# Performance work log

Hardware: AMD Instinct MI355X
Metric: run time of the kernel (lower is better)

## Reference

```python
import jax, jax.numpy as jnp
import numpy as np

LAM_CONSIST = 0.1
LAM_LR = 1.0
LAM_PAIR = 1.0


def _cubic(x, a=-0.75):
    # PyTorch bicubic kernel (a = -0.75)
    ax = jnp.abs(x)
    ax2 = ax * ax
    ax3 = ax2 * ax
    f1 = (a + 2.0) * ax3 - (a + 3.0) * ax2 + 1.0
    f2 = a * ax3 - 5.0 * a * ax2 + 8.0 * a * ax - 4.0 * a
    return jnp.where(ax <= 1.0, f1, jnp.where(ax < 2.0, f2, 0.0))


def _resize_matrix(in_size: int, out_size: int) -> jnp.ndarray:
    """Weight matrix [out_size, in_size] for antialiased bicubic resize
    (align_corners=False, antialias=True, border replicate) as in
    F.interpolate(..., mode='bicubic', antialias=True)."""
    scale = in_size / out_size
    s_aa = max(scale, 1.0)  # widen kernel when downscaling (antialias)
    support = 2.0 * s_aa
    ext = int(np.ceil(support)) + 1
    centers = (np.arange(out_size, dtype=np.float64) + 0.5) * scale - 0.5
    idx = np.arange(-ext, in_size + ext)
    dist = (idx[None, :] - centers[:, None]) / s_aa  # [out, in+2ext]
    w = _cubic(jnp.asarray(dist, dtype=jnp.float32))
    w = w / jnp.sum(w, axis=1, keepdims=True)  # torch normalizes window weights
    idx_c = np.clip(idx, 0, in_size - 1)  # clamp -> replicate border
    M = jnp.zeros((out_size, in_size), dtype=jnp.float32).at[:, idx_c].add(w)
    return M


def _resize_bicubic_aa(img: jnp.ndarray, th: int, tw: int) -> jnp.ndarray:
    # img: [B, C, H, W] -> [B, C, th, tw], separable resize via two matmuls
    _, _, h, w = img.shape
    Mh = _resize_matrix(h, th)  # [th, h]
    Mw = _resize_matrix(w, tw)  # [tw, w]
    return jnp.einsum('oh,bchw,pw->bcop', Mh, img, Mw)


def setup_inputs() -> dict:
    key = jax.random.key(0)
    k1, k2, k3 = jax.random.split(key, 3)
    pred_hr = jax.random.normal(k1, (32, 3, 512, 512), dtype=jnp.float32)
    target_hr = jax.random.normal(k2, (32, 3, 512, 512), dtype=jnp.float32)
    lr_ref = jax.random.normal(k3, (32, 3, 128, 128), dtype=jnp.float32)
    scale = jnp.full((32,), 4.0, dtype=jnp.float32)  # uniform -> static sizes
    return {"pred_hr": pred_hr, "target_hr": target_hr, "lr_ref": lr_ref, "scale": scale}


def reference(pred_hr, target_hr, lr_ref, scale):
    pix = jnp.mean(jnp.abs(pred_hr - target_hr))
    # project_scale(pred_hr, src=scale, dst=1): uniform scale=4 ->
    # target size == lr_ref spatial size (static, read from lr_ref shape)
    th, tw = lr_ref.shape[-2], lr_ref.shape[-1]
    pred_lr = _resize_bicubic_aa(pred_hr, th, tw)
    lr_term = jnp.mean(jnp.abs(pred_lr - lr_ref))
    pair_term = jnp.float32(0.0)  # pair_pred_hr / pair_scale are None
    consist = LAM_LR * lr_term + LAM_PAIR * pair_term
    total = pix + LAM_CONSIST * consist
    return (total, pix, consist, lr_term, pair_term)
```

## Files before the change

### kernel.cpp

```cpp
#include <hip/hip_runtime.h>

#define HW    512
#define OUTW  128
#define NIMG  96
#define N_HR  ((long long)NIMG*HW*HW)
#define N_LR  ((long long)NIMG*OUTW*OUTW)
#define NPART (NIMG*32)

__device__ __forceinline__ float cubic075(float x){
    float ax = fabsf(x);
    float ax2 = ax*ax, ax3 = ax2*ax;
    const float A = -0.75f;
    float f1 = (A+2.f)*ax3 - (A+3.f)*ax2 + 1.f;
    float f2 = A*ax3 - 5.f*A*ax2 + 8.f*A*ax - 4.f*A;
    return ax <= 1.f ? f1 : (ax < 2.f ? f2 : 0.f);
}

__device__ __forceinline__ void get_weights(float w[16]){
    float s = 0.f;
#pragma unroll
    for (int k = 0; k < 16; ++k){
        float d = ((float)k - 7.5f) * 0.25f;
        w[k] = cubic075(d);
        s += w[k];
    }
#pragma unroll
    for (int k = 0; k < 16; ++k) w[k] /= s;
}

__global__ __launch_bounds__(256) void kmain(const float* __restrict__ pred,
                                             const float* __restrict__ tgt,
                                             const float* __restrict__ lr,
                                             double* __restrict__ part){
    const int img = blockIdx.x >> 3;
    const int tid = threadIdx.x;
    const int w   = tid >> 6;
    const int l   = tid & 63;
    const int gw  = ((blockIdx.x & 7) << 2) + w;
    const int o0  = gw << 2;
    const int s   = (gw << 4) - 6;

    float wt[16]; get_weights(wt);
    const float* P = pred + (size_t)img * (HW*HW);
    const float* T = tgt  + (size_t)img * (HW*HW);
    const float* L = lr   + (size_t)img * (OUTW*OUTW);

    float acc[4][2] = {{0.f,0.f},{0.f,0.f},{0.f,0.f},{0.f,0.f}};
    float pix_acc = 0.f, lr_acc = 0.f;

    int r0 = min(HW-1, max(0, s + 0));
    int r1 = min(HW-1, max(0, s + 1));
    const float4* rp0 = (const float4*)(P + (size_t)r0 * HW);
    const float4* rp1 = (const float4*)(P + (size_t)r1 * HW);
    float4 c0 = rp0[2*l], c1 = rp0[2*l+1];
    float4 n0 = rp1[2*l], n1 = rp1[2*l+1];
    float4 tc0, tc1, tn0, tn1;

#pragma unroll 4
    for (int i = 0; i < 28; ++i){
        float4 f0, f1, tf0, tf1;
        if (i < 26){
            int rn = min(HW-1, max(0, s + i + 2));
            const float4* rp = (const float4*)(P + (size_t)rn * HW);
            f0 = rp[2*l]; f1 = rp[2*l+1];
        }
        if (i + 2 >= 6 && i + 2 < 22){
            const float4* tp = (const float4*)(T + (size_t)(s + i + 2) * HW);
            tf0 = tp[2*l]; tf1 = tp[2*l+1];
        }

        const float p0=c0.x,p1v=c0.y,p2v=c0.z,p3=c0.w,
                    p4=c1.x,p5=c1.y,p6=c1.z,p7=c1.w;

        if (i >= 6 && i < 22){
            pix_acc += fabsf(p0-tc0.x)+fabsf(p1v-tc0.y)+fabsf(p2v-tc0.z)+fabsf(p3-tc0.w)
                     + fabsf(p4-tc1.x)+fabsf(p5-tc1.y)+fabsf(p6-tc1.z)+fabsf(p7-tc1.w);
        }

        float Lm6 = __shfl_up(p2v,1,64), Lm5 = __shfl_up(p3,1,64),
              Lm4 = __shfl_up(p4,1,64),  Lm3 = __shfl_up(p5,1,64),
              Lm2 = __shfl_up(p6,1,64),  Lm1 = __shfl_up(p7,1,64);
        float R8  = __shfl_down(p0,1,64), R9  = __shfl_down(p1v,1,64),
              R10 = __shfl_down(p2v,1,64),R11 = __shfl_down(p3,1,64),
              R12 = __shfl_down(p4,1,64), R13 = __shfl_down(p5,1,64);
        if (l == 0){ Lm6=p0; Lm5=p0; Lm4=p0; Lm3=p0; Lm2=p0; Lm1=p0; }
        if (l == 63){ R8=p7; R9=p7; R10=p7; R11=p7; R12=p7; R13=p7; }

        float w20[20] = {Lm6,Lm5,Lm4,Lm3,Lm2,Lm1,p0,p1v,p2v,p3,p4,p5,p6,p7,
                         R8,R9,R10,R11,R12,R13};
        float h0 = 0.f, h1 = 0.f;
#pragma unroll
        for (int k = 0; k < 16; ++k){
            h0 += wt[k]*w20[k];
            h1 += wt[k]*w20[k+4];
        }

#pragma unroll
        for (int q = 0; q < 4; ++q){
            int k = i - 4*q;
            if (k >= 0 && k < 16){
                acc[q][0] += wt[k]*h0;
                acc[q][1] += wt[k]*h1;
            }
        }

        c0=n0; c1=n1; n0=f0; n1=f1;
        tc0=tn0; tc1=tn1; tn0=tf0; tn1=tf1;
    }

#pragma unroll
    for (int q = 0; q < 4; ++q){
        const float2 lv = *(const float2*)(L + (size_t)(o0+q)*OUTW + 2*l);
        lr_acc += fabsf(acc[q][0]-lv.x) + fabsf(acc[q][1]-lv.y);
    }

#pragma unroll
    for (int off = 32; off > 0; off >>= 1){
        pix_acc += __shfl_down(pix_acc, off, 64);
        lr_acc  += __shfl_down(lr_acc,  off, 64);
    }
    if (l == 0){
        const int slot = (blockIdx.x << 2) + w;
        part[slot]         = (double)pix_acc;
        part[NPART + slot] = (double)lr_acc;
    }
}

__global__ __launch_bounds__(256) void k3(const double* __restrict__ part,
                                          float* __restrict__ out){
    const int t = threadIdx.x;
    double v1 = 0.0, v2 = 0.0;
    for (int i = t; i < NPART; i += 256){
        v1 += part[i];
        v2 += part[NPART + i];
    }
#pragma unroll
    for (int off = 32; off > 0; off >>= 1){
        v1 += __shfl_down(v1, off, 64);
        v2 += __shfl_down(v2, off, 64);
    }
    __shared__ double s1[4], s2[4];
    const int lane = t & 63, wid = t >> 6;
    if (lane == 0){ s1[wid] = v1; s2[wid] = v2; }
    __syncthreads();
    if (t == 0){
        double S1 = s1[0]+s1[1]+s1[2]+s1[3];
        double S2 = s2[0]+s2[1]+s2[2]+s2[3];
        float pix     = (float)(S1 / (double)N_HR);
        float lr_term = (float)(S2 / (double)N_LR);
        float pair    = 0.f;
        float consist = 1.0f * lr_term + 1.0f * pair;
        float total   = pix + 0.1f * consist;
        out[0] = total; out[1] = pix; out[2] = consist; out[3] = lr_term; out[4] = pair;
    }
}

extern "C" void kernel_launch(void* const* d_in, const int* in_sizes, int n_in,
                              void* d_out, int out_size, void* d_ws, size_t ws_size,
                              hipStream_t stream){
    const float* pred = (const float*)d_in[0];
    const float* tgt  = (const float*)d_in[1];
    const float* lrr  = (const float*)d_in[2];
    float* out = (float*)d_out;

    double* part = (double*)d_ws;

    kmain<<<NIMG*8, 256, 0, stream>>>(pred, tgt, lrr, part);
    k3<<<1, 256, 0, stream>>>(part, out);
}
```

Measured before the change: 230.9 us.

## Stage pred/target rows through LDS ring via async global_load_lds

Replaces register double-buffering of input rows with a 3-slot per-wave LDS ring. Rows are filled by `__builtin_amdgcn_global_load_lds` direct-to-LDS loads, synchronised with explicit `s_waitcnt vmcnt` counts. The 28-row loop is now fully unrolled so the wait counts are compile-time constants. The aim is to keep more row loads in flight and free VGPRs, hiding memory latency in this bandwidth-starved kernel. The cost is 48KB of LDS per block, which can limit occupancy, and a reliance on hand-counted vmcnt values that must stay correct.

```diff
diff --git a/kernel.cpp b/kernel.cpp
--- a/kernel.cpp
+++ b/kernel.cpp
@@ -28,10 +28,33 @@
     for (int k = 0; k < 16; ++k) w[k] /= s;
 }
 
+__device__ __forceinline__ void gl16(const float* g, float* l){
+    __builtin_amdgcn_global_load_lds(
+        (const __attribute__((address_space(1))) void*)g,
+        (__attribute__((address_space(3))) void*)l,
+        16, 0, 0);
+}
+
+__device__ __forceinline__ void stage_row(const float* rowbase, float* ldsbase, int l){
+    gl16(rowbase + 4*l,       ldsbase);
+    gl16(rowbase + 4*l + 256, ldsbase + 256);
+}
+
+__device__ __forceinline__ void waitv(int n){
+    if (n >= 8)      asm volatile("s_waitcnt vmcnt(8)" ::: "memory");
+    else if (n == 6) asm volatile("s_waitcnt vmcnt(6)" ::: "memory");
+    else if (n == 4) asm volatile("s_waitcnt vmcnt(4)" ::: "memory");
+    else if (n == 2) asm volatile("s_waitcnt vmcnt(2)" ::: "memory");
+    else             asm volatile("s_waitcnt vmcnt(0)" ::: "memory");
+}
+
 __global__ __launch_bounds__(256) void kmain(const float* __restrict__ pred,
                                              const float* __restrict__ tgt,
                                              const float* __restrict__ lr,
                                              double* __restrict__ part){
+    __shared__ float ringP[4][3][512];
+    __shared__ float ringT[4][3][512];
+
     const int img = blockIdx.x >> 3;
     const int tid = threadIdx.x;
     const int w   = tid >> 6;
@@ -48,33 +71,37 @@
     float acc[4][2] = {{0.f,0.f},{0.f,0.f},{0.f,0.f},{0.f,0.f}};
     float pix_acc = 0.f, lr_acc = 0.f;
 
-    int r0 = min(HW-1, max(0, s + 0));
-    int r1 = min(HW-1, max(0, s + 1));
-    const float4* rp0 = (const float4*)(P + (size_t)r0 * HW);
-    const float4* rp1 = (const float4*)(P + (size_t)r1 * HW);
-    float4 c0 = rp0[2*l], c1 = rp0[2*l+1];
-    float4 n0 = rp1[2*l], n1 = rp1[2*l+1];
-    float4 tc0, tc1, tn0, tn1;
+    {
+        int r0 = min(HW-1, max(0, s + 0));
+        int r1 = min(HW-1, max(0, s + 1));
+        stage_row(P + (size_t)r0*HW, &ringP[w][0][0], l);
+        stage_row(P + (size_t)r1*HW, &ringP[w][1][0], l);
+    }
 
-#pragma unroll 4
+#pragma unroll
     for (int i = 0; i < 28; ++i){
-        float4 f0, f1, tf0, tf1;
-        if (i < 26){
-            int rn = min(HW-1, max(0, s + i + 2));
-            const float4* rp = (const float4*)(P + (size_t)rn * HW);
-            f0 = rp[2*l]; f1 = rp[2*l+1];
+        if (i + 2 < 28){
+            int rr = min(HW-1, max(0, s + i + 2));
+            stage_row(P + (size_t)rr*HW, &ringP[w][(i+2)%3][0], l);
         }
         if (i + 2 >= 6 && i + 2 < 22){
-            const float4* tp = (const float4*)(T + (size_t)(s + i + 2) * HW);
-            tf0 = tp[2*l]; tf1 = tp[2*l+1];
+            stage_row(T + (size_t)(s+i+2)*HW, &ringT[w][(i+2)%3][0], l);
         }
 
+        const int Ni = ((i+1<28)?2:0) + ((i+1>=6 && i+1<22)?2:0)
+                     + ((i+2<28)?2:0) + ((i+2>=6 && i+2<22)?2:0);
+        waitv(Ni);
+
+        const float4* pr = (const float4*)(&ringP[w][i%3][0]);
+        const float4 c0 = pr[2*l], c1 = pr[2*l+1];
         const float p0=c0.x,p1v=c0.y,p2v=c0.z,p3=c0.w,
                     p4=c1.x,p5=c1.y,p6=c1.z,p7=c1.w;
 
         if (i >= 6 && i < 22){
-            pix_acc += fabsf(p0-tc0.x)+fabsf(p1v-tc0.y)+fabsf(p2v-tc0.z)+fabsf(p3-tc0.w)
-                     + fabsf(p4-tc1.x)+fabsf(p5-tc1.y)+fabsf(p6-tc1.z)+fabsf(p7-tc1.w);
+            const float4* trp = (const float4*)(&ringT[w][i%3][0]);
+            const float4 t0 = trp[2*l], t1 = trp[2*l+1];
+            pix_acc += fabsf(p0-t0.x)+fabsf(p1v-t0.y)+fabsf(p2v-t0.z)+fabsf(p3-t0.w)
+                     + fabsf(p4-t1.x)+fabsf(p5-t1.y)+fabsf(p6-t1.z)+fabsf(p7-t1.w);
         }
 
         float Lm6 = __shfl_up(p2v,1,64), Lm5 = __shfl_up(p3,1,64),
@@ -97,15 +124,12 @@
 
 #pragma unroll
         for (int q = 0; q < 4; ++q){
-            int k = i - 4*q;
-            if (k >= 0 && k < 16){
-                acc[q][0] += wt[k]*h0;
-                acc[q][1] += wt[k]*h1;
+            int kk = i - 4*q;
+            if (kk >= 0 && kk < 16){
+                acc[q][0] += wt[kk]*h0;
+                acc[q][1] += wt[kk]*h1;
             }
         }
-
-        c0=n0; c1=n1; n0=f0; n1=f1;
-        tc0=tn0; tc1=tn1; tn0=tf0; tn1=tf1;
     }
 
 #pragma unroll
```

After: 228.1 us. No clear change (-1.2%).

## Stage pred/target rows into LDS via global_load_lds double-buffering shared across waves

Applied to the files above, without the earlier changes.

Replaces per-wave register row streaming with a block-wide double-buffered LDS pipeline fed by global_load_lds, so the four waves of a block share 4-row chunks of the input instead of each re-reading its own overlapping 28-row window. Each block now covers 64 consecutive output rows with sliding chunks, and blocks are remapped so that adjacent block IDs touch different images. This aims to cut redundant HBM/L2 traffic from overlapping vertical windows. In exchange it adds barriers every chunk, manual vmcnt waits and uneven per-wave work (each wave is active on only 7 of 19 chunks for the resize), which could hurt latency hiding.

```diff
diff --git a/kernel.cpp b/kernel.cpp
--- a/kernel.cpp
+++ b/kernel.cpp
@@ -28,17 +28,28 @@
     for (int k = 0; k < 16; ++k) w[k] /= s;
 }
 
+__device__ __forceinline__ void gl16(const float* g, float* l){
+    __builtin_amdgcn_global_load_lds(
+        (const __attribute__((address_space(1))) void*)g,
+        (__attribute__((address_space(3))) void*)l,
+        16, 0, 0);
+}
+
 __global__ __launch_bounds__(256) void kmain(const float* __restrict__ pred,
                                              const float* __restrict__ tgt,
                                              const float* __restrict__ lr,
                                              double* __restrict__ part){
-    const int img = blockIdx.x >> 3;
-    const int tid = threadIdx.x;
-    const int w   = tid >> 6;
-    const int l   = tid & 63;
-    const int gw  = ((blockIdx.x & 7) << 2) + w;
-    const int o0  = gw << 2;
-    const int s   = (gw << 4) - 6;
+    __shared__ float bufP[2][4][512];
+    __shared__ float bufT[2][4][512];
+
+    const int logical = ((blockIdx.x & 7) * 96) + (blockIdx.x >> 3);
+    const int img  = logical >> 3;
+    const int B    = logical & 7;
+    const int tid  = threadIdx.x;
+    const int w    = tid >> 6;
+    const int l    = tid & 63;
+    const int sblk = (B << 6) - 6;
+    const int o0   = (B << 4) + (w << 2);
 
     float wt[16]; get_weights(wt);
     const float* P = pred + (size_t)img * (HW*HW);
@@ -48,65 +59,91 @@
     float acc[4][2] = {{0.f,0.f},{0.f,0.f},{0.f,0.f},{0.f,0.f}};
     float pix_acc = 0.f, lr_acc = 0.f;
 
-    int r0 = min(HW-1, max(0, s + 0));
-    int r1 = min(HW-1, max(0, s + 1));
-    const float4* rp0 = (const float4*)(P + (size_t)r0 * HW);
-    const float4* rp1 = (const float4*)(P + (size_t)r1 * HW);
-    float4 c0 = rp0[2*l], c1 = rp0[2*l+1];
-    float4 n0 = rp1[2*l], n1 = rp1[2*l+1];
-    float4 tc0, tc1, tn0, tn1;
-
-#pragma unroll 4
-    for (int i = 0; i < 28; ++i){
-        float4 f0, f1, tf0, tf1;
-        if (i < 26){
-            int rn = min(HW-1, max(0, s + i + 2));
-            const float4* rp = (const float4*)(P + (size_t)rn * HW);
-            f0 = rp[2*l]; f1 = rp[2*l+1];
-        }
-        if (i + 2 >= 6 && i + 2 < 22){
-            const float4* tp = (const float4*)(T + (size_t)(s + i + 2) * HW);
-            tf0 = tp[2*l]; tf1 = tp[2*l+1];
-        }
-
-        const float p0=c0.x,p1v=c0.y,p2v=c0.z,p3=c0.w,
-                    p4=c1.x,p5=c1.y,p6=c1.z,p7=c1.w;
-
-        if (i >= 6 && i < 22){
-            pix_acc += fabsf(p0-tc0.x)+fabsf(p1v-tc0.y)+fabsf(p2v-tc0.z)+fabsf(p3-tc0.w)
-                     + fabsf(p4-tc1.x)+fabsf(p5-tc1.y)+fabsf(p6-tc1.z)+fabsf(p7-tc1.w);
-        }
-
-        float Lm6 = __shfl_up(p2v,1,64), Lm5 = __shfl_up(p3,1,64),
-              Lm4 = __shfl_up(p4,1,64),  Lm3 = __shfl_up(p5,1,64),
-              Lm2 = __shfl_up(p6,1,64),  Lm1 = __shfl_up(p7,1,64);
-        float R8  = __shfl_down(p0,1,64), R9  = __shfl_down(p1v,1,64),
-              R10 = __shfl_down(p2v,1,64),R11 = __shfl_down(p3,1,64),
-              R12 = __shfl_down(p4,1,64), R13 = __shfl_down(p5,1,64);
-        if (l == 0){ Lm6=p0; Lm5=p0; Lm4=p0; Lm3=p0; Lm2=p0; Lm1=p0; }
-        if (l == 63){ R8=p7; R9=p7; R10=p7; R11=p7; R12=p7; R13=p7; }
-
-        float w20[20] = {Lm6,Lm5,Lm4,Lm3,Lm2,Lm1,p0,p1v,p2v,p3,p4,p5,p6,p7,
-                         R8,R9,R10,R11,R12,R13};
-        float h0 = 0.f, h1 = 0.f;
-#pragma unroll
-        for (int k = 0; k < 16; ++k){
-            h0 += wt[k]*w20[k];
-            h1 += wt[k]*w20[k+4];
-        }
-
-#pragma unroll
-        for (int q = 0; q < 4; ++q){
-            int k = i - 4*q;
-            if (k >= 0 && k < 16){
-                acc[q][0] += wt[k]*h0;
-                acc[q][1] += wt[k]*h1;
+#define STAGE(cc) do{                                                          \
+    _Pragma("unroll")                                                          \
+    for (int j = 0; j < 2; ++j){                                               \
+        const int grp  = (j<<2) + w;                                           \
+        const int row  = grp >> 1;                                             \
+        const int half = grp & 1;                                              \
+        const int gP   = min(HW-1, max(0, sblk + ((cc)<<2) + row));            \
+        gl16(P + (size_t)gP*HW + half*256 + 4*l, &bufP[(cc)&1][row][half*256]);\
+        const int bic  = min(69, max(6, ((cc)<<2) + row));                     \
+        gl16(T + (size_t)(sblk+bic)*HW + half*256 + 4*l,                       \
+             &bufT[(cc)&1][row][half*256]);                                    \
+    }                                                                          \
+}while(0)
+
+#define VROW(k, r) do{                                                         \
+    if ((k) >= 0  && (k) < 16)  { acc[0][0]+=wt[(k)]   *h[r][0]; acc[0][1]+=wt[(k)]   *h[r][1]; } \
+    if ((k) >= 4  && (k) < 20)  { acc[1][0]+=wt[(k)-4] *h[r][0]; acc[1][1]+=wt[(k)-4] *h[r][1]; } \
+    if ((k) >= 8  && (k) < 24)  { acc[2][0]+=wt[(k)-8] *h[r][0]; acc[2][1]+=wt[(k)-8] *h[r][1]; } \
+    if ((k) >= 12 && (k) < 28)  { acc[3][0]+=wt[(k)-12]*h[r][0]; acc[3][1]+=wt[(k)-12]*h[r][1]; } \
+}while(0)
+
+    STAGE(0);
+
+#pragma unroll 1
+    for (int c = 0; c < 19; ++c){
+        STAGE(c+1);
+        asm volatile("s_waitcnt vmcnt(4)" ::: "memory");
+        __builtin_amdgcn_s_barrier();
+
+        {
+            const int rhi = w >> 1;
+            const int col = ((w & 1) << 6) + l;
+#pragma unroll
+            for (int j2 = 0; j2 < 2; ++j2){
+                const int row = (j2 << 1) + rhi;
+                const int bi  = (c << 2) + row;
+                if (bi >= 6 && bi < 70){
+                    const float4 pv = *(const float4*)&bufP[c&1][row][col<<2];
+                    const float4 tv = *(const float4*)&bufT[c&1][row][col<<2];
+                    pix_acc += fabsf(pv.x-tv.x)+fabsf(pv.y-tv.y)
+                             + fabsf(pv.z-tv.z)+fabsf(pv.w-tv.w);
+                }
             }
         }
 
-        c0=n0; c1=n1; n0=f0; n1=f1;
-        tc0=tn0; tc1=tn1; tn0=tf0; tn1=tf1;
-    }
+        const int m = c - (w << 2);
+        if (m >= 0 && m < 7){
+            float h[4][2];
+#pragma unroll
+            for (int r = 0; r < 4; ++r){
+                const float4* pr = (const float4*)&bufP[c&1][r][0];
+                const float4 c0 = pr[2*l], c1 = pr[2*l+1];
+                const float p0=c0.x,p1v=c0.y,p2v=c0.z,p3=c0.w,
+                            p4=c1.x,p5=c1.y,p6=c1.z,p7=c1.w;
+                float Lm6 = __shfl_up(p2v,1,64), Lm5 = __shfl_up(p3,1,64),
+                      Lm4 = __shfl_up(p4,1,64),  Lm3 = __shfl_up(p5,1,64),
+                      Lm2 = __shfl_up(p6,1,64),  Lm1 = __shfl_up(p7,1,64);
+                float R8  = __shfl_down(p0,1,64), R9  = __shfl_down(p1v,1,64),
+                      R10 = __shfl_down(p2v,1,64),R11 = __shfl_down(p3,1,64),
+                      R12 = __shfl_down(p4,1,64), R13 = __shfl_down(p5,1,64);
+                if (l == 0){ Lm6=p0; Lm5=p0; Lm4=p0; Lm3=p0; Lm2=p0; Lm1=p0; }
+                if (l == 63){ R8=p7; R9=p7; R10=p7; R11=p7; R12=p7; R13=p7; }
+                float w20[20] = {Lm6,Lm5,Lm4,Lm3,Lm2,Lm1,p0,p1v,p2v,p3,p4,p5,p6,p7,
+                                 R8,R9,R10,R11,R12,R13};
+                float h0 = 0.f, h1 = 0.f;
+#pragma unroll
+                for (int k = 0; k < 16; ++k){ h0 += wt[k]*w20[k]; h1 += wt[k]*w20[k+4]; }
+                h[r][0] = h0; h[r][1] = h1;
+            }
+            switch(m){
+                case 0: VROW(0,0);  VROW(1,1);  VROW(2,2);  VROW(3,3);  break;
+                case 1: VROW(4,0);  VROW(5,1);  VROW(6,2);  VROW(7,3);  break;
+                case 2: VROW(8,0);  VROW(9,1);  VROW(10,2); VROW(11,3); break;
+                case 3: VROW(12,0); VROW(13,1); VROW(14,2); VROW(15,3); break;
+                case 4: VROW(16,0); VROW(17,1); VROW(18,2); VROW(19,3); break;
+                case 5: VROW(20,0); VROW(21,1); VROW(22,2); VROW(23,3); break;
+                case 6: VROW(24,0); VROW(25,1); VROW(26,2); VROW(27,3); break;
+            }
+        }
+
+        __builtin_amdgcn_s_barrier();
+    }
+
+#undef VROW
+#undef STAGE
 
 #pragma unroll
     for (int q = 0; q < 4; ++q){
```

Result: slower. 235.6 us (+2.1%).
